# Performance work log

Hardware: AMD Instinct MI355X
Metric: run time of the kernel (lower is better)

## Reference

```python
import jax, jax.numpy as jnp
import numpy as np

B, N, D, NS, HID = 64, 4096, 256, 8, 512
ITERS = 3
EPS = 1e-08
SCALE = D ** -0.5
LN_EPS = 1e-5


def _layernorm(x, g, b):
    m = x.mean(-1, keepdims=True)
    v = ((x - m) ** 2).mean(-1, keepdims=True)
    return (x - m) * jax.lax.rsqrt(v + LN_EPS) * g + b


def setup_inputs() -> dict:
    key = jax.random.key(0)
    ks = jax.random.split(key, 20)
    s = 0.02
    return {
        "inputs": jax.random.normal(ks[0], (B, N, D), jnp.float32),
        "noise": jax.random.normal(ks[1], (B, NS, D), jnp.float32),
        "slots_mu": jax.random.normal(ks[2], (1, 1, D), jnp.float32),
        "slots_logsigma": jax.random.normal(ks[3], (1, 1, D), jnp.float32) * s,
        "Wq": jax.random.normal(ks[4], (D, D), jnp.float32) * s,  # (in, out): y = x @ Wq
        "Wk": jax.random.normal(ks[5], (D, D), jnp.float32) * s,
        "Wv": jax.random.normal(ks[6], (D, D), jnp.float32) * s,
        "gru_wi": jax.random.normal(ks[7], (3 * D, D), jnp.float32) * s,  # torch GRUCell weight_ih
        "gru_wh": jax.random.normal(ks[8], (3 * D, D), jnp.float32) * s,
        "gru_bi": jnp.zeros((3 * D,), jnp.float32),
        "gru_bh": jnp.zeros((3 * D,), jnp.float32),
        "mlp_w1": jax.random.normal(ks[9], (D, HID), jnp.float32) * s,
        "mlp_b1": jnp.zeros((HID,), jnp.float32),
        "mlp_w2": jax.random.normal(ks[10], (HID, D), jnp.float32) * s,
        "mlp_b2": jnp.zeros((D,), jnp.float32),
        "ln_in_g": jnp.ones((D,), jnp.float32),
        "ln_in_b": jnp.zeros((D,), jnp.float32),
        "ln_s_g": jnp.ones((D,), jnp.float32),
        "ln_s_b": jnp.zeros((D,), jnp.float32),
        "ln_ff_g": jnp.ones((D,), jnp.float32),
        "ln_ff_b": jnp.zeros((D,), jnp.float32),
    }


def _step(slots, k, v, Wq, gru_wi, gru_wh, gru_bi, gru_bh,
          mlp_w1, mlp_b1, mlp_w2, mlp_b2, ln_s_g, ln_s_b, ln_ff_g, ln_ff_b):
    b, ns, d = slots.shape
    slots_prev = slots
    q = _layernorm(slots, ln_s_g, ln_s_b) @ Wq                  # [b, ns, d]
    dots = jnp.einsum('bid,bjd->bij', q, k) * SCALE             # [b, ns, n]
    attn = jax.nn.softmax(dots, axis=1) + EPS                   # softmax over slot dim
    attn = attn / attn.sum(-1, keepdims=True)                   # renormalize over tokens
    updates = jnp.einsum('bjd,bij->bid', v, attn)               # [b, ns, d]
    # GRUCell (torch semantics)
    x = updates.reshape(-1, d)
    h = slots_prev.reshape(-1, d)
    gi = x @ gru_wi.T + gru_bi
    gh = h @ gru_wh.T + gru_bh
    ir, iz, inn = jnp.split(gi, 3, axis=-1)
    hr, hz, hn = jnp.split(gh, 3, axis=-1)
    r = jax.nn.sigmoid(ir + hr)
    z = jax.nn.sigmoid(iz + hz)
    nng = jnp.tanh(inn + r * hn)
    h_new = (1.0 - z) * nng + z * h
    slots = h_new.reshape(b, ns, d)
    ff = _layernorm(slots, ln_ff_g, ln_ff_b)
    slots = slots + jax.nn.relu(ff @ mlp_w1 + mlp_b1) @ mlp_w2 + mlp_b2
    return slots


def reference(inputs, noise, slots_mu, slots_logsigma, Wq, Wk, Wv,
              gru_wi, gru_wh, gru_bi, gru_bh,
              mlp_w1, mlp_b1, mlp_w2, mlp_b2,
              ln_in_g, ln_in_b, ln_s_g, ln_s_b, ln_ff_g, ln_ff_b):
    slots = slots_mu + jnp.exp(slots_logsigma) * noise          # [B, NS, D]
    x = _layernorm(inputs, ln_in_g, ln_in_b)
    k = x @ Wk
    v = x @ Wv
    args = (Wq, gru_wi, gru_wh, gru_bi, gru_bh, mlp_w1, mlp_b1, mlp_w2, mlp_b2,
            ln_s_g, ln_s_b, ln_ff_g, ln_ff_b)
    for _ in range(ITERS):
        slots = _step(slots, k, v, *args)
    slots = _step(jax.lax.stop_gradient(slots), k, v, *args)
    return slots
```

## Files before the change

### kernel.cpp

```cpp
#include <hip/hip_runtime.h>
#include <cstdint>

#define B_ 64
#define N_ 4096
#define D_ 256
#define NS_ 8
#define HID_ 512
#define TOK_ 128
#define NPART_ 32
#define EPS_ 1e-8f
#define SCALE_ 0.0625f
#define LN_EPS_ 1e-5f

typedef _Float16 f16;
typedef __attribute__((ext_vector_type(4))) _Float16 f16x4;
typedef __attribute__((ext_vector_type(8))) _Float16 f16x8;
typedef __attribute__((ext_vector_type(4))) float f32x4;

#define MFMA16(a, b, c) __builtin_amdgcn_mfma_f32_16x16x32_f16(a, b, c, 0, 0, 0)

__global__ __launch_bounds__(256) void k_setup(
    const float* __restrict__ in, const float* __restrict__ gin,
    const float* __restrict__ bin, f16* __restrict__ xh,
    const float* __restrict__ Wk, float* __restrict__ WkX,
    const float* __restrict__ wi, const float* __restrict__ wh,
    f16* __restrict__ wiTh, f16* __restrict__ whTh,
    const float* __restrict__ noise, const float* __restrict__ mu,
    const float* __restrict__ ls, float* __restrict__ slots,
    const float* __restrict__ w1, const float* __restrict__ w2,
    f16* __restrict__ w1h, f16* __restrict__ w2h) {
  const int blk = blockIdx.x;
  const int t = threadIdx.x;
  if (blk < 65536) {
    const int wave = t >> 6, lane = t & 63;
    const size_t row = (size_t)blk * 4 + wave;
    const float* r = in + row * D_;
    float4 a = *(const float4*)(r + lane * 4);
    float s1 = a.x + a.y + a.z + a.w;
    float s2 = a.x * a.x + a.y * a.y + a.z * a.z + a.w * a.w;
    #pragma unroll
    for (int m = 32; m >= 1; m >>= 1) { s1 += __shfl_xor(s1, m, 64); s2 += __shfl_xor(s2, m, 64); }
    const float mean = s1 * (1.f / D_);
    const float rstd = rsqrtf(s2 * (1.f / D_) - mean * mean + LN_EPS_);
    float4 gg = *(const float4*)(gin + lane * 4);
    float4 bv = *(const float4*)(bin + lane * 4);
    f16x4 o;
    o[0] = (f16)((a.x - mean) * rstd * gg.x + bv.x);
    o[1] = (f16)((a.y - mean) * rstd * gg.y + bv.y);
    o[2] = (f16)((a.z - mean) * rstd * gg.z + bv.z);
    o[3] = (f16)((a.w - mean) * rstd * gg.w + bv.w);
    *(f16x4*)(xh + row * D_ + lane * 4) = o;
  } else if (blk < 65792) {
    const int e = blk - 65536;
    WkX[t * 256 + e] = Wk[e * 256 + t];
  } else if (blk < 66560) {
    const int idx = (blk - 65792) * 256 + t;
    const int o = idx >> 8, d = idx & 255;
    wiTh[d * 768 + o] = (f16)wi[idx];
    whTh[d * 768 + o] = (f16)wh[idx];
  } else if (blk < 67072) {
    const int idx = (blk - 66560) * 256 + t;
    const int d = idx & 255;
    slots[idx] = mu[d] + __expf(ls[d]) * noise[idx];
  } else if (blk < 67584) {
    const int idx = (blk - 67072) * 256 + t;
    w1h[idx] = (f16)w1[idx];
  } else {
    const int idx = (blk - 67584) * 256 + t;
    w2h[idx] = (f16)w2[idx];
  }
}

__global__ __launch_bounds__(256) void k_m(const float* __restrict__ Wq,
                                           const float* __restrict__ WkX,
                                           float* __restrict__ M) {
  __shared__ float wq[256];
  const int c = blockIdx.x, e = threadIdx.x;
  wq[e] = Wq[c * 256 + e];
  __syncthreads();
  float a0 = 0.f, a1 = 0.f, a2 = 0.f, a3 = 0.f;
  #pragma unroll 8
  for (int d = 0; d < 256; d += 4) {
    a0 = fmaf(wq[d],     WkX[(d)     * 256 + e], a0);
    a1 = fmaf(wq[d + 1], WkX[(d + 1) * 256 + e], a1);
    a2 = fmaf(wq[d + 2], WkX[(d + 2) * 256 + e], a2);
    a3 = fmaf(wq[d + 3], WkX[(d + 3) * 256 + e], a3);
  }
  M[c * 256 + e] = (a0 + a1 + a2 + a3) * SCALE_;
}

__global__ __launch_bounds__(256) void k_qk(const float* __restrict__ slots,
    const float* __restrict__ g, const float* __restrict__ b,
    const float* __restrict__ M, f16* __restrict__ qkh) {
  const int row = blockIdx.x;
  const int t = threadIdx.x;
  __shared__ float sl[256];
  __shared__ float red1[4], red2[4];
  float val = slots[(size_t)row * D_ + t];
  float s1 = val, s2 = val * val;
  #pragma unroll
  for (int m = 32; m >= 1; m >>= 1) { s1 += __shfl_xor(s1, m, 64); s2 += __shfl_xor(s2, m, 64); }
  int wave = t >> 6, lane = t & 63;
  if (lane == 0) { red1[wave] = s1; red2[wave] = s2; }
  __syncthreads();
  s1 = red1[0] + red1[1] + red1[2] + red1[3];
  s2 = red2[0] + red2[1] + red2[2] + red2[3];
  float mean = s1 * (1.f / D_);
  float rstd = rsqrtf(s2 * (1.f / D_) - mean * mean + LN_EPS_);
  sl[t] = (val - mean) * rstd * g[t] + b[t];
  __syncthreads();
  float a0 = 0.f, a1 = 0.f, a2 = 0.f, a3 = 0.f;
  #pragma unroll 8
  for (int d = 0; d < D_; d += 4) {
    a0 = fmaf(sl[d],     M[(d)     * D_ + t], a0);
    a1 = fmaf(sl[d + 1], M[(d + 1) * D_ + t], a1);
    a2 = fmaf(sl[d + 2], M[(d + 2) * D_ + t], a2);
    a3 = fmaf(sl[d + 3], M[(d + 3) * D_ + t], a3);
  }
  qkh[((size_t)(row >> 3) * 16 + (row & 7)) * D_ + t] = (f16)(a0 + a1 + a2 + a3);
}

__global__ __launch_bounds__(512) void k_attn_upd(
    const f16* __restrict__ xh, const f16* __restrict__ qkh,
    float* __restrict__ urp, float* __restrict__ asp) {
  __shared__ __align__(16) f16 xt[TOK_ * 256];
  __shared__ __align__(16) f16 qs[16 * 256];
  __shared__ float wv_s[TOK_ * 12];
  const int b = blockIdx.y;
  const int blkx = blockIdx.x;
  const int jt = blkx * TOK_;
  const int part = b * NPART_ + blkx;
  const int tid = threadIdx.x;
  const int wave = tid >> 6, lane = tid & 63;

  {
    const int r = tid >> 5, c = tid & 31;
    const f16* src = qkh + ((size_t)b * 16 + r) * D_;
    *(f16x8*)&qs[r * 256 + (c ^ (r & 7)) * 8] = *(const f16x8*)(src + c * 8);
  }
  {
    const f16* src = xh + ((size_t)b * N_ + jt) * D_;
    f16x8 v[8];
    #pragma unroll
    for (int i = 0; i < 8; ++i) {
      const int r = i * 16 + (tid >> 5), c = tid & 31;
      v[i] = *(const f16x8*)(src + r * 256 + c * 8);
    }
    #pragma unroll
    for (int i = 0; i < 8; ++i) {
      const int r = i * 16 + (tid >> 5), c = tid & 31;
      *(f16x8*)&xt[r * 256 + (c ^ (r & 7)) * 8] = v[i];
    }
  }
  __syncthreads();

  const int kg = lane >> 4;
  f16x8 afr[8];
  {
    const int arow = lane & 15;
    #pragma unroll
    for (int kk = 0; kk < 8; ++kk)
      afr[kk] = *(const f16x8*)&qs[arow * 256 + ((kk * 4 + kg) ^ (arow & 7)) * 8];
  }
  {
    const int tok = wave * 16 + (lane & 15);
    f32x4 acc = {0.f, 0.f, 0.f, 0.f};
    #pragma unroll
    for (int kk = 0; kk < 8; ++kk) {
      f16x8 bf = *(const f16x8*)&xt[tok * 256 + ((kk * 4 + kg) ^ (tok & 7)) * 8];
      acc = MFMA16(afr[kk], bf, acc);
    }
    float o0 = __shfl_xor(acc[0], 16, 64);
    float o1 = __shfl_xor(acc[1], 16, 64);
    float o2 = __shfl_xor(acc[2], 16, 64);
    float o3 = __shfl_xor(acc[3], 16, 64);
    if (lane < 32) {
      float m = fmaxf(fmaxf(fmaxf(acc[0], acc[1]), fmaxf(acc[2], acc[3])),
                      fmaxf(fmaxf(o0, o1), fmaxf(o2, o3)));
      float e0 = __expf(acc[0] - m), e1 = __expf(acc[1] - m);
      float e2 = __expf(acc[2] - m), e3 = __expf(acc[3] - m);
      float sm = e0 + e1 + e2 + e3;
      float so = __shfl_xor(sm, 16, 64);
      float inv = 1.f / (sm + so);
      float4 wv;
      wv.x = e0 * inv + EPS_; wv.y = e1 * inv + EPS_;
      wv.z = e2 * inv + EPS_; wv.w = e3 * inv + EPS_;
      *(float4*)&wv_s[tok * 12 + (lane >> 4) * 4] = wv;
    }
  }
  __syncthreads();

  {
    const int ch0 = lane >> 1, sub = (lane & 1) * 4;
    float a0[4] = {0.f, 0.f, 0.f, 0.f};
    float s0 = 0.f;
    #pragma unroll 4
    for (int j = 0; j < TOK_; ++j) {
      f16x4 v = *(const f16x4*)&xt[j * 256 + (ch0 ^ (j & 7)) * 8 + sub];
      float w0 = wv_s[j * 12 + wave];
      s0 += w0;
      a0[0] = fmaf(w0, (float)v[0], a0[0]);
      a0[1] = fmaf(w0, (float)v[1], a0[1]);
      a0[2] = fmaf(w0, (float)v[2], a0[2]);
      a0[3] = fmaf(w0, (float)v[3], a0[3]);
    }
    *(float4*)(urp + ((size_t)part * NS_ + wave) * D_ + lane * 4) =
        make_float4(a0[0], a0[1], a0[2], a0[3]);
    if (lane == 0) asp[part * NS_ + wave] = s0;
  }
}

__global__ __launch_bounds__(512) void k_gru_mlp(
    const float* __restrict__ urp, const float* __restrict__ asp,
    const float* __restrict__ slots, const float* __restrict__ Wv,
    const f16* __restrict__ wiTh, const f16* __restrict__ whTh,
    const float* __restrict__ bi, const float* __restrict__ bh,
    const f16* __restrict__ w1h, const float* __restrict__ b1,
    const f16* __restrict__ w2h, const float* __restrict__ b2,
    const float* __restrict__ gf, const float* __restrict__ bf,
    const float* __restrict__ gs, const float* __restrict__ bs,
    const float* __restrict__ M,
    float* __restrict__ out, f16* __restrict__ qkh) {
  const int row = blockIdx.x;
  const int bb = row >> 3, ii = row & 7;
  const int t = threadIdx.x;
  const int half = t >> 8;
  const int tl = t & 255;
  const int wave = t >> 6, lane = t & 63;
  __shared__ float urs[256], xs[256], hs[256], ffs[256], hid[512], hn_s[256];
  __shared__ float p2[2][256];
  __shared__ float part[6][512];
  __shared__ float red1[8], red2[8];

  {
    float usum = 0.f;
    #pragma unroll
    for (int p = half * 16; p < half * 16 + 16; ++p)
      usum += urp[((size_t)(bb * NPART_ + p) * NS_ + ii) * D_ + tl];
    p2[half][tl] = usum;
  }
  if (t < 256) hs[tl] = slots[(size_t)row * D_ + tl];
  {
    float ap = (t < NPART_) ? asp[(size_t)(bb * NPART_ + t) * NS_ + ii] : 0.f;
    if (wave == 0) {
      #pragma unroll
      for (int m = 32; m >= 1; m >>= 1) ap += __shfl_xor(ap, m, 64);
      if (t == 0) red1[0] = ap;
    }
  }
  __syncthreads();
  if (t < 256) urs[tl] = p2[0][tl] + p2[1][tl];
  const float asv = red1[0];
  __syncthreads();

  {
    float u0 = 0.f, u1 = 0.f;
    const int e0 = half * 128;
    #pragma unroll 8
    for (int e = e0; e < e0 + 128; e += 2) {
      u0 = fmaf(urs[e],     Wv[(size_t)(e)     * D_ + tl], u0);
      u1 = fmaf(urs[e + 1], Wv[(size_t)(e + 1) * D_ + tl], u1);
    }
    p2[half][tl] = u0 + u1;
  }
  __syncthreads();
  if (t < 256) xs[tl] = (p2[0][tl] + p2[1][tl]) / asv;
  __syncthreads();

  {
    float a0 = 0.f, a1 = 0.f, a2 = 0.f, a3 = 0.f, a4 = 0.f, a5 = 0.f;
    const int d0 = half * 128;
    #pragma unroll 4
    for (int d = d0; d < d0 + 128; ++d) {
      const f16* wid = wiTh + d * 768;
      const f16* whd = whTh + d * 768;
      float xd = xs[d], hd = hs[d];
      a0 = fmaf(xd, (float)wid[tl], a0);
      a1 = fmaf(xd, (float)wid[D_ + tl], a1);
      a2 = fmaf(xd, (float)wid[2 * D_ + tl], a2);
      a3 = fmaf(hd, (float)whd[tl], a3);
      a4 = fmaf(hd, (float)whd[D_ + tl], a4);
      a5 = fmaf(hd, (float)whd[2 * D_ + tl], a5);
    }
    part[0][t] = a0; part[1][t] = a1; part[2][t] = a2;
    part[3][t] = a3; part[4][t] = a4; part[5][t] = a5;
  }
  __syncthreads();
  float hnew = 0.f;
  if (t < 256) {
    float gi0 = bi[tl]          + part[0][tl] + part[0][256 + tl];
    float gi1 = bi[D_ + tl]     + part[1][tl] + part[1][256 + tl];
    float gi2 = bi[2 * D_ + tl] + part[2][tl] + part[2][256 + tl];
    float gh0 = bh[tl]          + part[3][tl] + part[3][256 + tl];
    float gh1 = bh[D_ + tl]     + part[4][tl] + part[4][256 + tl];
    float gh2 = bh[2 * D_ + tl] + part[5][tl] + part[5][256 + tl];
    float r = 1.f / (1.f + __expf(-(gi0 + gh0)));
    float z = 1.f / (1.f + __expf(-(gi1 + gh1)));
    float n = tanhf(gi2 + r * gh2);
    hnew = (1.f - z) * n + z * hs[tl];
    hn_s[tl] = hnew;
  }
  {
    float v = (t < 256) ? hnew : 0.f;
    float s1 = v, s2 = v * v;
    #pragma unroll
    for (int m = 32; m >= 1; m >>= 1) { s1 += __shfl_xor(s1, m, 64); s2 += __shfl_xor(s2, m, 64); }
    if (lane == 0) { red1[wave] = s1; red2[wave] = s2; }
    __syncthreads();
    float ts1 = 0.f, ts2 = 0.f;
    #pragma unroll
    for (int w = 0; w < 8; ++w) { ts1 += red1[w]; ts2 += red2[w]; }
    float mean = ts1 * (1.f / D_);
    float rstd = rsqrtf(ts2 * (1.f / D_) - mean * mean + LN_EPS_);
    if (t < 256) ffs[tl] = (hnew - mean) * rstd * gf[tl] + bf[tl];
  }
  __syncthreads();
  {
    float h = b1[t];
    #pragma unroll 8
    for (int d = 0; d < D_; ++d)
      h = fmaf(ffs[d], (float)w1h[(size_t)d * HID_ + t], h);
    hid[t] = fmaxf(h, 0.f);
  }
  __syncthreads();
  {
    float o0 = 0.f, o1 = 0.f;
    const int d0 = half * 256;
    #pragma unroll 8
    for (int d = d0; d < d0 + 256; d += 2) {
      o0 = fmaf(hid[d],     (float)w2h[(size_t)(d)     * D_ + tl], o0);
      o1 = fmaf(hid[d + 1], (float)w2h[(size_t)(d + 1) * D_ + tl], o1);
    }
    p2[half][tl] = o0 + o1;
  }
  __syncthreads();
  float o = 0.f;
  if (t < 256) {
    o = b2[tl] + p2[0][tl] + p2[1][tl] + hn_s[tl];
    out[(size_t)row * D_ + tl] = o;
  }
  {
    float v = (t < 256) ? o : 0.f;
    float s1 = v, s2 = v * v;
    #pragma unroll
    for (int m = 32; m >= 1; m >>= 1) { s1 += __shfl_xor(s1, m, 64); s2 += __shfl_xor(s2, m, 64); }
    __syncthreads();
    if (lane == 0) { red1[wave] = s1; red2[wave] = s2; }
    __syncthreads();
    float ts1 = 0.f, ts2 = 0.f;
    #pragma unroll
    for (int w = 0; w < 8; ++w) { ts1 += red1[w]; ts2 += red2[w]; }
    float mean = ts1 * (1.f / D_);
    float rstd = rsqrtf(ts2 * (1.f / D_) - mean * mean + LN_EPS_);
    if (t < 256) ffs[tl] = (o - mean) * rstd * gs[tl] + bs[tl];
  }
  __syncthreads();
  {
    float a0 = 0.f, a1 = 0.f;
    const int d0 = half * 128;
    #pragma unroll 8
    for (int d = d0; d < d0 + 128; d += 2) {
      a0 = fmaf(ffs[d],     M[(d)     * D_ + tl], a0);
      a1 = fmaf(ffs[d + 1], M[(d + 1) * D_ + tl], a1);
    }
    p2[half][tl] = a0 + a1;
  }
  __syncthreads();
  if (t < 256)
    qkh[((size_t)bb * 16 + ii) * D_ + tl] = (f16)(p2[0][tl] + p2[1][tl]);
}

extern "C" void kernel_launch(void* const* d_in, const int* in_sizes, int n_in,
                              void* d_out, int out_size, void* d_ws, size_t ws_size,
                              hipStream_t stream) {
  (void)in_sizes; (void)n_in; (void)out_size; (void)ws_size;
  const float* inputs = (const float*)d_in[0];
  const float* noise  = (const float*)d_in[1];
  const float* mu     = (const float*)d_in[2];
  const float* ls     = (const float*)d_in[3];
  const float* Wq     = (const float*)d_in[4];
  const float* Wk     = (const float*)d_in[5];
  const float* Wv     = (const float*)d_in[6];
  const float* gwi    = (const float*)d_in[7];
  const float* gwh    = (const float*)d_in[8];
  const float* gbi    = (const float*)d_in[9];
  const float* gbh    = (const float*)d_in[10];
  const float* w1     = (const float*)d_in[11];
  const float* b1     = (const float*)d_in[12];
  const float* w2     = (const float*)d_in[13];
  const float* b2     = (const float*)d_in[14];
  const float* gin    = (const float*)d_in[15];
  const float* bin    = (const float*)d_in[16];
  const float* gs     = (const float*)d_in[17];
  const float* bs     = (const float*)d_in[18];
  const float* gff    = (const float*)d_in[19];
  const float* bff    = (const float*)d_in[20];

  const size_t KV = (size_t)B_ * N_ * D_;
  f16*   xh    = (f16*)d_ws;
  float* slots = (float*)(xh + KV);
  f16*   qkh   = (f16*)(slots + 131072);
  float* asp   = (float*)(qkh + 262144);
  float* urp   = asp + 16384;
  float* WkX   = urp + (size_t)B_ * NPART_ * NS_ * D_;
  float* M     = WkX + 65536;
  f16*   wiTh  = (f16*)(M + 65536);
  f16*   whTh  = wiTh + 196608;
  f16*   w1h   = whTh + 196608;
  f16*   w2h   = w1h + 131072;

  k_setup<<<68096, 256, 0, stream>>>(inputs, gin, bin, xh, Wk, WkX,
                                     gwi, gwh, wiTh, whTh,
                                     noise, mu, ls, slots, w1, w2, w1h, w2h);
  k_m<<<256, 256, 0, stream>>>(Wq, WkX, M);
  k_qk<<<512, 256, 0, stream>>>(slots, gs, bs, M, qkh);
  for (int it = 0; it < 4; ++it) {
    k_attn_upd<<<dim3(NPART_, B_), 512, 0, stream>>>(xh, qkh, urp, asp);
    float* outp = (it == 3) ? (float*)d_out : slots;
    k_gru_mlp<<<512, 512, 0, stream>>>(urp, asp, slots, Wv, wiTh, whTh, gbi, gbh,
                                       w1h, b1, w2h, b2, gff, bff, gs, bs, M,
                                       outp, qkh);
  }
}
```

Baseline: 494.3 us.

## Process all slots of a batch per block in GRU/MLP kernel to reuse weights

The GRU/MLP/query-projection kernel now runs one block per batch element instead of one per slot row. Each thread accumulates 4 (or 8) slot rows at once, so each weight element loaded from global memory is reused across rows. This removes redundant weight reads but reduces grid size from 512 to 64 blocks, lowering GPU occupancy and lengthening per-block serial work.

```diff
diff --git a/kernel.cpp b/kernel.cpp
--- a/kernel.cpp
+++ b/kernel.cpp
@@ -221,153 +221,169 @@
     const float* __restrict__ gs, const float* __restrict__ bs,
     const float* __restrict__ M,
     float* __restrict__ out, f16* __restrict__ qkh) {
-  const int row = blockIdx.x;
-  const int bb = row >> 3, ii = row & 7;
+  const int bb = blockIdx.x;
   const int t = threadIdx.x;
-  const int half = t >> 8;
-  const int tl = t & 255;
+  const int half = t >> 8, tl = t & 255;
+  const int rbase = half * 4;
   const int wave = t >> 6, lane = t & 63;
-  __shared__ float urs[256], xs[256], hs[256], ffs[256], hid[512], hn_s[256];
-  __shared__ float p2[2][256];
-  __shared__ float part[6][512];
-  __shared__ float red1[8], red2[8];
-
-  {
-    float usum = 0.f;
-    #pragma unroll
-    for (int p = half * 16; p < half * 16 + 16; ++p)
-      usum += urp[((size_t)(bb * NPART_ + p) * NS_ + ii) * D_ + tl];
-    p2[half][tl] = usum;
-  }
-  if (t < 256) hs[tl] = slots[(size_t)row * D_ + tl];
-  {
-    float ap = (t < NPART_) ? asp[(size_t)(bb * NPART_ + t) * NS_ + ii] : 0.f;
-    if (wave == 0) {
-      #pragma unroll
-      for (int m = 32; m >= 1; m >>= 1) ap += __shfl_xor(ap, m, 64);
-      if (t == 0) red1[0] = ap;
-    }
-  }
-  __syncthreads();
-  if (t < 256) urs[tl] = p2[0][tl] + p2[1][tl];
-  const float asv = red1[0];
-  __syncthreads();
-
-  {
-    float u0 = 0.f, u1 = 0.f;
-    const int e0 = half * 128;
+  const int wl = wave & 3;
+  __shared__ float urs[8][256], xs[8][256], hs[8][256], ffs[8][256];
+  __shared__ float hid[8][512];
+  __shared__ float as_s[8];
+  __shared__ float red1[8][4], red2[8][4];
+
+  #pragma unroll
+  for (int c = t; c < 2048; c += 512) {
+    const int ii = c >> 8, d = c & 255;
+    float s = 0.f;
     #pragma unroll 8
-    for (int e = e0; e < e0 + 128; e += 2) {
-      u0 = fmaf(urs[e],     Wv[(size_t)(e)     * D_ + tl], u0);
-      u1 = fmaf(urs[e + 1], Wv[(size_t)(e + 1) * D_ + tl], u1);
-    }
-    p2[half][tl] = u0 + u1;
-  }
-  __syncthreads();
-  if (t < 256) xs[tl] = (p2[0][tl] + p2[1][tl]) / asv;
-  __syncthreads();
-
-  {
-    float a0 = 0.f, a1 = 0.f, a2 = 0.f, a3 = 0.f, a4 = 0.f, a5 = 0.f;
-    const int d0 = half * 128;
+    for (int p = 0; p < NPART_; ++p)
+      s += urp[((size_t)(bb * NPART_ + p) * NS_ + ii) * D_ + d];
+    urs[ii][d] = s;
+  }
+  #pragma unroll
+  for (int c = t; c < 2048; c += 512)
+    hs[c >> 8][c & 255] = slots[(size_t)bb * 2048 + c];
+  if (t < 256) {
+    float ap = asp[(size_t)(bb * NPART_ + (t >> 3)) * NS_ + (t & 7)];
+    ap += __shfl_xor(ap, 8, 64);
+    ap += __shfl_xor(ap, 16, 64);
+    ap += __shfl_xor(ap, 32, 64);
+    if (lane < 8) red1[lane][wave] = ap;
+  }
+  __syncthreads();
+  if (t < 8) as_s[t] = red1[t][0] + red1[t][1] + red1[t][2] + red1[t][3];
+  __syncthreads();
+
+  {
+    float a0 = 0.f, a1 = 0.f, a2 = 0.f, a3 = 0.f;
     #pragma unroll 4
-    for (int d = d0; d < d0 + 128; ++d) {
+    for (int e = 0; e < D_; ++e) {
+      float w = Wv[(size_t)e * D_ + tl];
+      a0 = fmaf(urs[rbase + 0][e], w, a0);
+      a1 = fmaf(urs[rbase + 1][e], w, a1);
+      a2 = fmaf(urs[rbase + 2][e], w, a2);
+      a3 = fmaf(urs[rbase + 3][e], w, a3);
+    }
+    xs[rbase + 0][tl] = a0 / as_s[rbase + 0];
+    xs[rbase + 1][tl] = a1 / as_s[rbase + 1];
+    xs[rbase + 2][tl] = a2 / as_s[rbase + 2];
+    xs[rbase + 3][tl] = a3 / as_s[rbase + 3];
+  }
+  __syncthreads();
+
+  float gi0[4], gi1[4], gi2[4], gh0[4], gh1[4], gh2[4];
+  {
+    const float b0 = bi[tl], b1v = bi[D_ + tl], b2v = bi[2 * D_ + tl];
+    const float c0 = bh[tl], c1v = bh[D_ + tl], c2v = bh[2 * D_ + tl];
+    #pragma unroll
+    for (int r = 0; r < 4; ++r) {
+      gi0[r] = b0; gi1[r] = b1v; gi2[r] = b2v;
+      gh0[r] = c0; gh1[r] = c1v; gh2[r] = c2v;
+    }
+    #pragma unroll 2
+    for (int d = 0; d < D_; ++d) {
       const f16* wid = wiTh + d * 768;
       const f16* whd = whTh + d * 768;
-      float xd = xs[d], hd = hs[d];
-      a0 = fmaf(xd, (float)wid[tl], a0);
-      a1 = fmaf(xd, (float)wid[D_ + tl], a1);
-      a2 = fmaf(xd, (float)wid[2 * D_ + tl], a2);
-      a3 = fmaf(hd, (float)whd[tl], a3);
-      a4 = fmaf(hd, (float)whd[D_ + tl], a4);
-      a5 = fmaf(hd, (float)whd[2 * D_ + tl], a5);
-    }
-    part[0][t] = a0; part[1][t] = a1; part[2][t] = a2;
-    part[3][t] = a3; part[4][t] = a4; part[5][t] = a5;
-  }
-  __syncthreads();
-  float hnew = 0.f;
-  if (t < 256) {
-    float gi0 = bi[tl]          + part[0][tl] + part[0][256 + tl];
-    float gi1 = bi[D_ + tl]     + part[1][tl] + part[1][256 + tl];
-    float gi2 = bi[2 * D_ + tl] + part[2][tl] + part[2][256 + tl];
-    float gh0 = bh[tl]          + part[3][tl] + part[3][256 + tl];
-    float gh1 = bh[D_ + tl]     + part[4][tl] + part[4][256 + tl];
-    float gh2 = bh[2 * D_ + tl] + part[5][tl] + part[5][256 + tl];
-    float r = 1.f / (1.f + __expf(-(gi0 + gh0)));
-    float z = 1.f / (1.f + __expf(-(gi1 + gh1)));
-    float n = tanhf(gi2 + r * gh2);
-    hnew = (1.f - z) * n + z * hs[tl];
-    hn_s[tl] = hnew;
-  }
-  {
-    float v = (t < 256) ? hnew : 0.f;
-    float s1 = v, s2 = v * v;
+      float wA = (float)wid[tl], wB = (float)wid[D_ + tl], wC = (float)wid[2 * D_ + tl];
+      float vA = (float)whd[tl], vB = (float)whd[D_ + tl], vC = (float)whd[2 * D_ + tl];
+      #pragma unroll
+      for (int r = 0; r < 4; ++r) {
+        float xd = xs[rbase + r][d], hd = hs[rbase + r][d];
+        gi0[r] = fmaf(xd, wA, gi0[r]);
+        gi1[r] = fmaf(xd, wB, gi1[r]);
+        gi2[r] = fmaf(xd, wC, gi2[r]);
+        gh0[r] = fmaf(hd, vA, gh0[r]);
+        gh1[r] = fmaf(hd, vB, gh1[r]);
+        gh2[r] = fmaf(hd, vC, gh2[r]);
+      }
+    }
+  }
+  float hnew[4];
+  #pragma unroll
+  for (int r = 0; r < 4; ++r) {
+    float rr = 1.f / (1.f + __expf(-(gi0[r] + gh0[r])));
+    float zz = 1.f / (1.f + __expf(-(gi1[r] + gh1[r])));
+    float nn = tanhf(gi2[r] + rr * gh2[r]);
+    hnew[r] = (1.f - zz) * nn + zz * hs[rbase + r][tl];
+  }
+  #pragma unroll
+  for (int r = 0; r < 4; ++r) {
+    float s1 = hnew[r], s2 = hnew[r] * hnew[r];
     #pragma unroll
     for (int m = 32; m >= 1; m >>= 1) { s1 += __shfl_xor(s1, m, 64); s2 += __shfl_xor(s2, m, 64); }
-    if (lane == 0) { red1[wave] = s1; red2[wave] = s2; }
-    __syncthreads();
-    float ts1 = 0.f, ts2 = 0.f;
-    #pragma unroll
-    for (int w = 0; w < 8; ++w) { ts1 += red1[w]; ts2 += red2[w]; }
-    float mean = ts1 * (1.f / D_);
-    float rstd = rsqrtf(ts2 * (1.f / D_) - mean * mean + LN_EPS_);
-    if (t < 256) ffs[tl] = (hnew - mean) * rstd * gf[tl] + bf[tl];
-  }
-  __syncthreads();
-  {
-    float h = b1[t];
-    #pragma unroll 8
-    for (int d = 0; d < D_; ++d)
-      h = fmaf(ffs[d], (float)w1h[(size_t)d * HID_ + t], h);
-    hid[t] = fmaxf(h, 0.f);
-  }
-  __syncthreads();
-  {
-    float o0 = 0.f, o1 = 0.f;
-    const int d0 = half * 256;
-    #pragma unroll 8
-    for (int d = d0; d < d0 + 256; d += 2) {
-      o0 = fmaf(hid[d],     (float)w2h[(size_t)(d)     * D_ + tl], o0);
-      o1 = fmaf(hid[d + 1], (float)w2h[(size_t)(d + 1) * D_ + tl], o1);
-    }
-    p2[half][tl] = o0 + o1;
-  }
-  __syncthreads();
-  float o = 0.f;
-  if (t < 256) {
-    o = b2[tl] + p2[0][tl] + p2[1][tl] + hn_s[tl];
-    out[(size_t)row * D_ + tl] = o;
-  }
-  {
-    float v = (t < 256) ? o : 0.f;
-    float s1 = v, s2 = v * v;
+    if (lane == 0) { red1[rbase + r][wl] = s1; red2[rbase + r][wl] = s2; }
+  }
+  __syncthreads();
+  #pragma unroll
+  for (int r = 0; r < 4; ++r) {
+    float s1 = red1[rbase + r][0] + red1[rbase + r][1] + red1[rbase + r][2] + red1[rbase + r][3];
+    float s2 = red2[rbase + r][0] + red2[rbase + r][1] + red2[rbase + r][2] + red2[rbase + r][3];
+    float mean = s1 * (1.f / D_);
+    float rstd = rsqrtf(s2 * (1.f / D_) - mean * mean + LN_EPS_);
+    ffs[rbase + r][tl] = (hnew[r] - mean) * rstd * gf[tl] + bf[tl];
+  }
+  __syncthreads();
+  {
+    float acc[8];
+    const float bv = b1[t];
+    #pragma unroll
+    for (int r = 0; r < 8; ++r) acc[r] = bv;
+    #pragma unroll 4
+    for (int d = 0; d < D_; ++d) {
+      float w = (float)w1h[(size_t)d * HID_ + t];
+      #pragma unroll
+      for (int r = 0; r < 8; ++r) acc[r] = fmaf(ffs[r][d], w, acc[r]);
+    }
+    #pragma unroll
+    for (int r = 0; r < 8; ++r) hid[r][t] = fmaxf(acc[r], 0.f);
+  }
+  __syncthreads();
+  float o[4];
+  {
+    float acc[4] = {0.f, 0.f, 0.f, 0.f};
+    #pragma unroll 4
+    for (int d = 0; d < HID_; ++d) {
+      float w = (float)w2h[(size_t)d * D_ + tl];
+      #pragma unroll
+      for (int r = 0; r < 4; ++r) acc[r] = fmaf(hid[rbase + r][d], w, acc[r]);
+    }
+    const float bv = b2[tl];
+    #pragma unroll
+    for (int r = 0; r < 4; ++r) {
+      o[r] = bv + acc[r] + hnew[r];
+      out[((size_t)bb * NS_ + rbase + r) * D_ + tl] = o[r];
+    }
+  }
+  #pragma unroll
+  for (int r = 0; r < 4; ++r) {
+    float s1 = o[r], s2 = o[r] * o[r];
     #pragma unroll
     for (int m = 32; m >= 1; m >>= 1) { s1 += __shfl_xor(s1, m, 64); s2 += __shfl_xor(s2, m, 64); }
-    __syncthreads();
-    if (lane == 0) { red1[wave] = s1; red2[wave] = s2; }
-    __syncthreads();
-    float ts1 = 0.f, ts2 = 0.f;
-    #pragma unroll
-    for (int w = 0; w < 8; ++w) { ts1 += red1[w]; ts2 += red2[w]; }
-    float mean = ts1 * (1.f / D_);
-    float rstd = rsqrtf(ts2 * (1.f / D_) - mean * mean + LN_EPS_);
-    if (t < 256) ffs[tl] = (o - mean) * rstd * gs[tl] + bs[tl];
-  }
-  __syncthreads();
-  {
-    float a0 = 0.f, a1 = 0.f;
-    const int d0 = half * 128;
-    #pragma unroll 8
-    for (int d = d0; d < d0 + 128; d += 2) {
-      a0 = fmaf(ffs[d],     M[(d)     * D_ + tl], a0);
-      a1 = fmaf(ffs[d + 1], M[(d + 1) * D_ + tl], a1);
-    }
-    p2[half][tl] = a0 + a1;
-  }
-  __syncthreads();
-  if (t < 256)
-    qkh[((size_t)bb * 16 + ii) * D_ + tl] = (f16)(p2[0][tl] + p2[1][tl]);
+    if (lane == 0) { red1[rbase + r][wl] = s1; red2[rbase + r][wl] = s2; }
+  }
+  __syncthreads();
+  #pragma unroll
+  for (int r = 0; r < 4; ++r) {
+    float s1 = red1[rbase + r][0] + red1[rbase + r][1] + red1[rbase + r][2] + red1[rbase + r][3];
+    float s2 = red2[rbase + r][0] + red2[rbase + r][1] + red2[rbase + r][2] + red2[rbase + r][3];
+    float mean = s1 * (1.f / D_);
+    float rstd = rsqrtf(s2 * (1.f / D_) - mean * mean + LN_EPS_);
+    ffs[rbase + r][tl] = (o[r] - mean) * rstd * gs[tl] + bs[tl];
+  }
+  __syncthreads();
+  {
+    float acc[4] = {0.f, 0.f, 0.f, 0.f};
+    #pragma unroll 4
+    for (int d = 0; d < D_; ++d) {
+      float w = M[(size_t)d * D_ + tl];
+      #pragma unroll
+      for (int r = 0; r < 4; ++r) acc[r] = fmaf(ffs[rbase + r][d], w, acc[r]);
+    }
+    #pragma unroll
+    for (int r = 0; r < 4; ++r)
+      qkh[((size_t)bb * 16 + rbase + r) * D_ + tl] = (f16)acc[r];
+  }
 }
 
 extern "C" void kernel_launch(void* const* d_in, const int* in_sizes, int n_in,
@@ -417,8 +433,8 @@
   for (int it = 0; it < 4; ++it) {
     k_attn_upd<<<dim3(NPART_, B_), 512, 0, stream>>>(xh, qkh, urp, asp);
     float* outp = (it == 3) ? (float*)d_out : slots;
-    k_gru_mlp<<<512, 512, 0, stream>>>(urp, asp, slots, Wv, wiTh, whTh, gbi, gbh,
-                                       w1h, b1, w2h, b2, gff, bff, gs, bs, M,
-                                       outp, qkh);
-  }
-}
+    k_gru_mlp<<<B_, 512, 0, stream>>>(urp, asp, slots, Wv, wiTh, whTh, gbi, gbh,
+                                      w1h, b1, w2h, b2, gff, bff, gs, bs, M,
+                                      outp, qkh);
+  }
+}
```

Measured after the change: 860.8 us. 1.74x slower.
